# Performance work log

Measured on AMD Instinct MI355X. Metric: run time of the kernel, lower is better.

## Reference

```python
import jax, jax.numpy as jnp
import numpy as np

SEQ_LEN = 4096
INPUT_DIM = 768
DIM = 512
NUM_HEADS = 8
HEAD_DIM = DIM // NUM_HEADS
WINDOW_SIZE = 7
DILATION = 8
HALF_WINDOW = WINDOW_SIZE // 2  # 3
BIDIRECTIONAL = True


def _dilated_mask(seq_len):
    # allowed neighbors of query i: j = i + k*DILATION for k in [-HALF_WINDOW, HALF_WINDOW]
    # (only k<=0 if not bidirectional), clipped to [0, seq_len)
    idx = jnp.arange(seq_len)
    d = idx[None, :] - idx[:, None]  # j - i
    allowed = (d % DILATION == 0) & (jnp.abs(d) <= DILATION * HALF_WINDOW)
    if not BIDIRECTIONAL:
        allowed = allowed & (d <= 0)
    return jnp.where(allowed, 0.0, -jnp.inf).astype(jnp.float32)  # [S, S]


def setup_inputs() -> dict:
    key = jax.random.key(0)
    ks = jax.random.split(key, 6)
    s = 0.02
    return {
        "x": jax.random.normal(ks[0], (SEQ_LEN, INPUT_DIM), dtype=jnp.float32),
        "W_in": jax.random.normal(ks[1], (INPUT_DIM, DIM), dtype=jnp.float32) * s,
        "b_in": jnp.zeros((DIM,), dtype=jnp.float32),
        "W_tse": jax.random.normal(ks[2], (DIM, 3 * DIM), dtype=jnp.float32) * s,
        "W_out": jax.random.normal(ks[3], (DIM, DIM), dtype=jnp.float32) * s,
        "b_out": jnp.zeros((DIM,), dtype=jnp.float32),
    }


def reference(x, W_in, b_in, W_tse, W_out, b_out):
    S = x.shape[0]
    scale = HEAD_DIM ** -0.5
    h = x @ W_in + b_in                                   # [S, DIM]
    tse = (h @ W_tse).reshape(S, 3, NUM_HEADS, HEAD_DIM)   # [S, 3, H, hd]
    q, k, v = tse[:, 0], tse[:, 1], tse[:, 2]              # each [S, H, hd]
    scores = jnp.einsum("shd,thd->hst", q, k) * scale      # [H, S, S]
    scores = scores + _dilated_mask(S)[None, :, :]
    attn = jax.nn.softmax(scores, axis=-1)                 # [H, S, S]
    out = jnp.einsum("hst,thd->shd", attn, v)              # [S, H, hd]
    out = out.reshape(S, DIM)
    return out @ W_out + b_out                              # [S, DIM]
```

## Files before the change

kernel.cpp:

```cpp
#include <hip/hip_runtime.h>
#include <hip/hip_bf16.h>

#define S_LEN 4096
#define IN_DIM 768
#define D_DIM 512
#define N_HEADS 8
#define H_DIM 64
#define TSE_DIM 1536

typedef __attribute__((ext_vector_type(8))) short frag8;
typedef __attribute__((ext_vector_type(4))) float f32x4;

__device__ __forceinline__ unsigned short f2bfbits(float f) {
    unsigned int u = __float_as_uint(f);
    unsigned int r = (u + 0x7FFFu + ((u >> 16) & 1u)) >> 16;
    return (unsigned short)r;
}
__device__ __forceinline__ float bf2f(unsigned short b) {
    return __uint_as_float(((unsigned int)b) << 16);
}

__device__ __forceinline__ void gload_lds16(const void* g, void* l) {
    __builtin_amdgcn_global_load_lds(
        (const __attribute__((address_space(1))) unsigned int*)g,
        (__attribute__((address_space(3))) unsigned int*)l,
        16, 0, 0);
}

__global__ __launch_bounds__(256) void prep_kernel(
        const float4* __restrict__ x4, ushort4* __restrict__ xb4,
        const float* __restrict__ W_in,  unsigned short* __restrict__ WinT,
        const float* __restrict__ W_tse, unsigned short* __restrict__ WtseT,
        const float* __restrict__ W_out, unsigned short* __restrict__ WoutT) {
    __shared__ float tile[32][33];
    int b = blockIdx.x;
    if (b < 3072) {
        int i = b * 256 + threadIdx.x;
        float4 v = x4[i];
        ushort4 o;
        o.x = f2bfbits(v.x); o.y = f2bfbits(v.y);
        o.z = f2bfbits(v.z); o.w = f2bfbits(v.w);
        xb4[i] = o;
        return;
    }
    const float* in; unsigned short* out; int K, N, t;
    if (b < 3456)      { t = b - 3072; in = W_in;  out = WinT;  K = IN_DIM; N = D_DIM;  }
    else if (b < 4224) { t = b - 3456; in = W_tse; out = WtseT; K = D_DIM;  N = TSE_DIM;}
    else               { t = b - 4224; in = W_out; out = WoutT; K = D_DIM;  N = D_DIM;  }
    int ktiles = K / 32;
    int kb = (t % ktiles) * 32, nb = (t / ktiles) * 32;
    int tx = threadIdx.x & 31, ty = threadIdx.x >> 5;
    #pragma unroll
    for (int r = ty; r < 32; r += 8)
        tile[r][tx] = in[(size_t)(kb + r) * N + nb + tx];
    __syncthreads();
    #pragma unroll
    for (int r = ty; r < 32; r += 8)
        out[(size_t)(nb + r) * K + kb + tx] = f2bfbits(tile[tx][r]);
}

template<int NF, bool OUT_BF16, bool BIAS>
__global__ __launch_bounds__(256) void gemm_nt(
        const unsigned short* __restrict__ A,
        const unsigned short* __restrict__ Bt,
        const float* __restrict__ bias,
        void* __restrict__ C,
        int M, int N, int K) {
    constexpr int BN = 32 * NF;
    constexpr int BI = NF / 2;
    __shared__ __align__(16) unsigned short As[128 * 32];
    __shared__ __align__(16) unsigned short Bs[BN * 32];

    const int bm = blockIdx.x * 128;
    const int bn = blockIdx.y * BN;
    const int tid  = threadIdx.x;
    const int lane = tid & 63;
    const int wave = tid >> 6;
    const int wr = wave >> 1;
    const int wc = wave & 1;
    const int fr = lane & 15;
    const int fg = lane >> 4;

    const int srow = lane >> 2;
    const int scol = (lane & 3) * 8;

    const unsigned short* agp0 = A + (size_t)(bm + wave * 32 + srow) * K + scol;
    const unsigned short* agp1 = agp0 + (size_t)16 * K;
    unsigned short* alp0 = &As[(wave * 2) * 512];
    unsigned short* alp1 = alp0 + 512;

    const unsigned short* bgp[BI];
    unsigned short* blp[BI];
    #pragma unroll
    for (int r = 0; r < BI; ++r) {
        int ch = wave * BI + r;
        bgp[r] = Bt + (size_t)(bn + ch * 16 + srow) * K + scol;
        blp[r] = &Bs[ch * 512];
    }

    f32x4 acc[4][NF];
    #pragma unroll
    for (int mi = 0; mi < 4; ++mi)
        #pragma unroll
        for (int ni = 0; ni < NF; ++ni)
            acc[mi][ni] = (f32x4)(0.f);

    const int kTiles = K >> 5;
    for (int kt = 0; kt < kTiles; ++kt) {
        const int ko = kt << 5;
        gload_lds16(agp0 + ko, alp0);
        gload_lds16(agp1 + ko, alp1);
        #pragma unroll
        for (int r = 0; r < BI; ++r)
            gload_lds16(bgp[r] + ko, blp[r]);
        __syncthreads();

        frag8 a[4], b[NF];
        #pragma unroll
        for (int mi = 0; mi < 4; ++mi)
            a[mi] = *(const frag8*)&As[(wr * 64 + mi * 16 + fr) * 32 + fg * 8];
        #pragma unroll
        for (int ni = 0; ni < NF; ++ni)
            b[ni] = *(const frag8*)&Bs[(wc * (BN / 2) + ni * 16 + fr) * 32 + fg * 8];

        #pragma unroll
        for (int mi = 0; mi < 4; ++mi)
            #pragma unroll
            for (int ni = 0; ni < NF; ++ni)
                acc[mi][ni] = __builtin_amdgcn_mfma_f32_16x16x32_bf16(
                        a[mi], b[ni], acc[mi][ni], 0, 0, 0);
        __syncthreads();
    }

    #pragma unroll
    for (int mi = 0; mi < 4; ++mi) {
        int grow = bm + wr * 64 + mi * 16 + fg * 4;
        #pragma unroll
        for (int ni = 0; ni < NF; ++ni) {
            int gcol = bn + wc * (BN / 2) + ni * 16 + fr;
            float bv = BIAS ? bias[gcol] : 0.f;
            #pragma unroll
            for (int r = 0; r < 4; ++r) {
                float v = acc[mi][ni][r] + bv;
                if (OUT_BF16)
                    ((unsigned short*)C)[(size_t)(grow + r) * N + gcol] = f2bfbits(v);
                else
                    ((float*)C)[(size_t)(grow + r) * N + gcol] = v;
            }
        }
    }
}

__global__ __launch_bounds__(256) void attn_kernel(
        const unsigned short* __restrict__ tse, unsigned short* __restrict__ out) {
    const int s    = blockIdx.x * 4 + (threadIdx.x >> 6);
    const int lane = threadIdx.x & 63;
    const int off  = (lane >> 3) * H_DIM + (lane & 7) * 8;

    float qf[8];
    {
        frag8 q = *(const frag8*)(tse + (size_t)s * TSE_DIM + off);
        #pragma unroll
        for (int i = 0; i < 8; ++i) qf[i] = bf2f((unsigned short)q[i]);
    }

    float sc[7];
    #pragma unroll
    for (int j = 0; j < 7; ++j) {
        int t = s + (j - 3) * 8;
        bool valid = (t >= 0) && (t < S_LEN);
        float p = 0.f;
        if (valid) {
            frag8 k = *(const frag8*)(tse + (size_t)t * TSE_DIM + D_DIM + off);
            #pragma unroll
            for (int i = 0; i < 8; ++i) p += qf[i] * bf2f((unsigned short)k[i]);
        }
        p += __shfl_xor(p, 1, 64);
        p += __shfl_xor(p, 2, 64);
        p += __shfl_xor(p, 4, 64);
        sc[j] = valid ? p * 0.125f : -__builtin_inff();
    }

    float m = sc[0];
    #pragma unroll
    for (int j = 1; j < 7; ++j) m = fmaxf(m, sc[j]);

    float w[7], denom = 0.f;
    #pragma unroll
    for (int j = 0; j < 7; ++j) {
        w[j] = (sc[j] == -__builtin_inff()) ? 0.f : __expf(sc[j] - m);
        denom += w[j];
    }
    const float inv = 1.f / denom;

    float of[8];
    #pragma unroll
    for (int i = 0; i < 8; ++i) of[i] = 0.f;
    #pragma unroll
    for (int j = 0; j < 7; ++j) {
        int t = s + (j - 3) * 8;
        if (t >= 0 && t < S_LEN) {
            frag8 v = *(const frag8*)(tse + (size_t)t * TSE_DIM + 2 * D_DIM + off);
            #pragma unroll
            for (int i = 0; i < 8; ++i) of[i] += w[j] * bf2f((unsigned short)v[i]);
        }
    }

    frag8 o;
    #pragma unroll
    for (int i = 0; i < 8; ++i) o[i] = (short)f2bfbits(of[i] * inv);
    *(frag8*)(out + (size_t)s * D_DIM + off) = o;
}

extern "C" void kernel_launch(void* const* d_in, const int* in_sizes, int n_in,
                              void* d_out, int out_size, void* d_ws, size_t ws_size,
                              hipStream_t stream) {
    (void)in_sizes; (void)n_in; (void)out_size;
    const float* x     = (const float*)d_in[0];
    const float* W_in  = (const float*)d_in[1];
    const float* b_in  = (const float*)d_in[2];
    const float* W_tse = (const float*)d_in[3];
    const float* W_out = (const float*)d_in[4];
    const float* b_out = (const float*)d_in[5];

    char* p = (char*)d_ws;
    unsigned short* xb    = (unsigned short*)p; p += (size_t)S_LEN * IN_DIM * 2;
    unsigned short* WinT  = (unsigned short*)p; p += (size_t)D_DIM * IN_DIM * 2;
    unsigned short* WtseT = (unsigned short*)p; p += (size_t)TSE_DIM * D_DIM * 2;
    unsigned short* WoutT = (unsigned short*)p; p += (size_t)D_DIM * D_DIM * 2;
    unsigned short* h     = (unsigned short*)p; p += (size_t)S_LEN * D_DIM * 2;
    unsigned short* tse   = (unsigned short*)p; p += (size_t)S_LEN * TSE_DIM * 2;
    unsigned short* attn  = (unsigned short*)p; p += (size_t)S_LEN * D_DIM * 2;
    if ((size_t)(p - (char*)d_ws) > ws_size) return;

    prep_kernel<<<4480, 256, 0, stream>>>(
            (const float4*)x, (ushort4*)xb, W_in, WinT, W_tse, WtseT, W_out, WoutT);

    gemm_nt<2, true, true><<<dim3(S_LEN / 128, D_DIM / 64), 256, 0, stream>>>(
            xb, WinT, b_in, h, S_LEN, D_DIM, IN_DIM);
    gemm_nt<4, true, false><<<dim3(S_LEN / 128, TSE_DIM / 128), 256, 0, stream>>>(
            h, WtseT, nullptr, tse, S_LEN, TSE_DIM, D_DIM);
    attn_kernel<<<S_LEN / 4, 256, 0, stream>>>(tse, attn);
    gemm_nt<2, false, true><<<dim3(S_LEN / 128, D_DIM / 64), 256, 0, stream>>>(
            attn, WoutT, b_out, (float*)d_out, S_LEN, D_DIM, D_DIM);
}
```

Before: 62.74 us.

## Use 64x64 GEMM tiles with double-buffered LDS prefetch

Replaces the templated 128xBN GEMM with a fixed 64x64 tile whose LDS buffers are double-buffered, so the global-to-LDS load of the next K tile is issued before the MFMAs on the current one. Smaller tiles give more blocks to fill the many CUs for these modest sizes (512 blocks for the 512-wide GEMMs), and there is one barrier per K step instead of two. The cost is less reuse per block: more global and L2 traffic and fewer MFMAs per loaded byte. Correctness relies on the barrier at the end of each iteration both making the prefetched tile visible and stopping the other buffer from being overwritten while it is still being read.

```diff
diff --git a/kernel.cpp b/kernel.cpp
--- a/kernel.cpp
+++ b/kernel.cpp
@@ -59,23 +59,20 @@
         out[(size_t)(nb + r) * K + kb + tx] = f2bfbits(tile[tx][r]);
 }
 
-template<int NF, bool OUT_BF16, bool BIAS>
+template<bool OUT_BF16, bool BIAS>
 __global__ __launch_bounds__(256) void gemm_nt(
         const unsigned short* __restrict__ A,
         const unsigned short* __restrict__ Bt,
         const float* __restrict__ bias,
         void* __restrict__ C,
         int M, int N, int K) {
-    constexpr int BN = 32 * NF;
-    constexpr int BI = NF / 2;
-    __shared__ __align__(16) unsigned short As[128 * 32];
-    __shared__ __align__(16) unsigned short Bs[BN * 32];
-
-    const int bm = blockIdx.x * 128;
-    const int bn = blockIdx.y * BN;
-    const int tid  = threadIdx.x;
-    const int lane = tid & 63;
-    const int wave = tid >> 6;
+    __shared__ __align__(16) unsigned short As[2][64 * 32];
+    __shared__ __align__(16) unsigned short Bs[2][64 * 32];
+
+    const int bm = blockIdx.x * 64;
+    const int bn = blockIdx.y * 64;
+    const int lane = threadIdx.x & 63;
+    const int wave = threadIdx.x >> 6;
     const int wr = wave >> 1;
     const int wc = wave & 1;
     const int fr = lane & 15;
@@ -84,60 +81,72 @@
     const int srow = lane >> 2;
     const int scol = (lane & 3) * 8;
 
-    const unsigned short* agp0 = A + (size_t)(bm + wave * 32 + srow) * K + scol;
-    const unsigned short* agp1 = agp0 + (size_t)16 * K;
-    unsigned short* alp0 = &As[(wave * 2) * 512];
-    unsigned short* alp1 = alp0 + 512;
-
-    const unsigned short* bgp[BI];
-    unsigned short* blp[BI];
-    #pragma unroll
-    for (int r = 0; r < BI; ++r) {
-        int ch = wave * BI + r;
-        bgp[r] = Bt + (size_t)(bn + ch * 16 + srow) * K + scol;
-        blp[r] = &Bs[ch * 512];
-    }
-
-    f32x4 acc[4][NF];
-    #pragma unroll
-    for (int mi = 0; mi < 4; ++mi)
-        #pragma unroll
-        for (int ni = 0; ni < NF; ++ni)
+    const unsigned short* agp = A  + (size_t)(bm + wave * 16 + srow) * K + scol;
+    const unsigned short* bgp = Bt + (size_t)(bn + wave * 16 + srow) * K + scol;
+    unsigned short* alp0 = &As[0][wave * 512];
+    unsigned short* blp0 = &Bs[0][wave * 512];
+    unsigned short* alp1 = &As[1][wave * 512];
+    unsigned short* blp1 = &Bs[1][wave * 512];
+
+    f32x4 acc[2][2];
+    #pragma unroll
+    for (int mi = 0; mi < 2; ++mi)
+        #pragma unroll
+        for (int ni = 0; ni < 2; ++ni)
             acc[mi][ni] = (f32x4)(0.f);
 
-    const int kTiles = K >> 5;
-    for (int kt = 0; kt < kTiles; ++kt) {
-        const int ko = kt << 5;
-        gload_lds16(agp0 + ko, alp0);
-        gload_lds16(agp1 + ko, alp1);
-        #pragma unroll
-        for (int r = 0; r < BI; ++r)
-            gload_lds16(bgp[r] + ko, blp[r]);
-        __syncthreads();
-
-        frag8 a[4], b[NF];
-        #pragma unroll
-        for (int mi = 0; mi < 4; ++mi)
-            a[mi] = *(const frag8*)&As[(wr * 64 + mi * 16 + fr) * 32 + fg * 8];
-        #pragma unroll
-        for (int ni = 0; ni < NF; ++ni)
-            b[ni] = *(const frag8*)&Bs[(wc * (BN / 2) + ni * 16 + fr) * 32 + fg * 8];
-
-        #pragma unroll
-        for (int mi = 0; mi < 4; ++mi)
-            #pragma unroll
-            for (int ni = 0; ni < NF; ++ni)
+    const int nt = K >> 5;
+
+    gload_lds16(agp, alp0);
+    gload_lds16(bgp, blp0);
+    __syncthreads();
+
+    int cur = 0;
+    for (int kt = 0; kt + 1 < nt; ++kt) {
+        const int ko = (kt + 1) << 5;
+        gload_lds16(agp + ko, cur ? alp0 : alp1);
+        gload_lds16(bgp + ko, cur ? blp0 : blp1);
+
+        frag8 a[2], b[2];
+        #pragma unroll
+        for (int mi = 0; mi < 2; ++mi)
+            a[mi] = *(const frag8*)&As[cur][(wr * 32 + mi * 16 + fr) * 32 + fg * 8];
+        #pragma unroll
+        for (int ni = 0; ni < 2; ++ni)
+            b[ni] = *(const frag8*)&Bs[cur][(wc * 32 + ni * 16 + fr) * 32 + fg * 8];
+        #pragma unroll
+        for (int mi = 0; mi < 2; ++mi)
+            #pragma unroll
+            for (int ni = 0; ni < 2; ++ni)
                 acc[mi][ni] = __builtin_amdgcn_mfma_f32_16x16x32_bf16(
                         a[mi], b[ni], acc[mi][ni], 0, 0, 0);
+
         __syncthreads();
-    }
-
-    #pragma unroll
-    for (int mi = 0; mi < 4; ++mi) {
-        int grow = bm + wr * 64 + mi * 16 + fg * 4;
-        #pragma unroll
-        for (int ni = 0; ni < NF; ++ni) {
-            int gcol = bn + wc * (BN / 2) + ni * 16 + fr;
+        cur ^= 1;
+    }
+
+    {
+        frag8 a[2], b[2];
+        #pragma unroll
+        for (int mi = 0; mi < 2; ++mi)
+            a[mi] = *(const frag8*)&As[cur][(wr * 32 + mi * 16 + fr) * 32 + fg * 8];
+        #pragma unroll
+        for (int ni = 0; ni < 2; ++ni)
+            b[ni] = *(const frag8*)&Bs[cur][(wc * 32 + ni * 16 + fr) * 32 + fg * 8];
+        #pragma unroll
+        for (int mi = 0; mi < 2; ++mi)
+            #pragma unroll
+            for (int ni = 0; ni < 2; ++ni)
+                acc[mi][ni] = __builtin_amdgcn_mfma_f32_16x16x32_bf16(
+                        a[mi], b[ni], acc[mi][ni], 0, 0, 0);
+    }
+
+    #pragma unroll
+    for (int mi = 0; mi < 2; ++mi) {
+        int grow = bm + wr * 32 + mi * 16 + fg * 4;
+        #pragma unroll
+        for (int ni = 0; ni < 2; ++ni) {
+            int gcol = bn + wc * 32 + ni * 16 + fr;
             float bv = BIAS ? bias[gcol] : 0.f;
             #pragma unroll
             for (int r = 0; r < 4; ++r) {
@@ -236,11 +245,11 @@
     prep_kernel<<<4480, 256, 0, stream>>>(
             (const float4*)x, (ushort4*)xb, W_in, WinT, W_tse, WtseT, W_out, WoutT);
 
-    gemm_nt<2, true, true><<<dim3(S_LEN / 128, D_DIM / 64), 256, 0, stream>>>(
+    gemm_nt<true, true><<<dim3(S_LEN / 64, D_DIM / 64), 256, 0, stream>>>(
             xb, WinT, b_in, h, S_LEN, D_DIM, IN_DIM);
-    gemm_nt<4, true, false><<<dim3(S_LEN / 128, TSE_DIM / 128), 256, 0, stream>>>(
+    gemm_nt<true, false><<<dim3(S_LEN / 64, TSE_DIM / 64), 256, 0, stream>>>(
             h, WtseT, nullptr, tse, S_LEN, TSE_DIM, D_DIM);
     attn_kernel<<<S_LEN / 4, 256, 0, stream>>>(tse, attn);
-    gemm_nt<2, false, true><<<dim3(S_LEN / 128, D_DIM / 64), 256, 0, stream>>>(
+    gemm_nt<false, true><<<dim3(S_LEN / 64, D_DIM / 64), 256, 0, stream>>>(
             attn, WoutT, b_out, (float*)d_out, S_LEN, D_DIM, D_DIM);
 }
```

Result: faster. 53.03 us (-15.5%).

## Double-buffer GEMM LDS tiles and shrink block tiles for more blocks

Applied to the files above, without the earlier changes.

The GEMM kernel now keeps two LDS buffers and issues the global-to-LDS loads for the next K tile before running MFMAs on the current one, so there is one barrier per iteration instead of two. The M tile is also a template parameter. The 768- and 512-K GEMMs now use 64x64 tiles and the QKV GEMM uses 128x64, which raises the block count from 256-384 to 512-768 to fill the CUs better. The cost is more LDS per block, less operand reuse per block, and more redundant global traffic.

```diff
diff --git a/kernel.cpp b/kernel.cpp
--- a/kernel.cpp
+++ b/kernel.cpp
@@ -59,23 +59,23 @@
         out[(size_t)(nb + r) * K + kb + tx] = f2bfbits(tile[tx][r]);
 }
 
-template<int NF, bool OUT_BF16, bool BIAS>
+template<int MF, int NF, bool OUT_BF16, bool BIAS>
 __global__ __launch_bounds__(256) void gemm_nt(
         const unsigned short* __restrict__ A,
         const unsigned short* __restrict__ Bt,
         const float* __restrict__ bias,
         void* __restrict__ C,
         int M, int N, int K) {
-    constexpr int BN = 32 * NF;
+    constexpr int BM = MF * 32, BN = NF * 32;
+    constexpr int AI = MF / 2;
     constexpr int BI = NF / 2;
-    __shared__ __align__(16) unsigned short As[128 * 32];
-    __shared__ __align__(16) unsigned short Bs[BN * 32];
-
-    const int bm = blockIdx.x * 128;
+    __shared__ __align__(16) unsigned short As[2][BM * 32];
+    __shared__ __align__(16) unsigned short Bs[2][BN * 32];
+
+    const int bm = blockIdx.x * BM;
     const int bn = blockIdx.y * BN;
-    const int tid  = threadIdx.x;
-    const int lane = tid & 63;
-    const int wave = tid >> 6;
+    const int lane = threadIdx.x & 63;
+    const int wave = threadIdx.x >> 6;
     const int wr = wave >> 1;
     const int wc = wave & 1;
     const int fr = lane & 15;
@@ -84,57 +84,78 @@
     const int srow = lane >> 2;
     const int scol = (lane & 3) * 8;
 
-    const unsigned short* agp0 = A + (size_t)(bm + wave * 32 + srow) * K + scol;
-    const unsigned short* agp1 = agp0 + (size_t)16 * K;
-    unsigned short* alp0 = &As[(wave * 2) * 512];
-    unsigned short* alp1 = alp0 + 512;
-
+    const unsigned short* agp[AI];
     const unsigned short* bgp[BI];
-    unsigned short* blp[BI];
-    #pragma unroll
-    for (int r = 0; r < BI; ++r) {
-        int ch = wave * BI + r;
-        bgp[r] = Bt + (size_t)(bn + ch * 16 + srow) * K + scol;
-        blp[r] = &Bs[ch * 512];
-    }
-
-    f32x4 acc[4][NF];
-    #pragma unroll
-    for (int mi = 0; mi < 4; ++mi)
+    #pragma unroll
+    for (int r = 0; r < AI; ++r)
+        agp[r] = A + (size_t)(bm + (wave * AI + r) * 16 + srow) * K + scol;
+    #pragma unroll
+    for (int r = 0; r < BI; ++r)
+        bgp[r] = Bt + (size_t)(bn + (wave * BI + r) * 16 + srow) * K + scol;
+
+    f32x4 acc[MF][NF];
+    #pragma unroll
+    for (int mi = 0; mi < MF; ++mi)
         #pragma unroll
         for (int ni = 0; ni < NF; ++ni)
             acc[mi][ni] = (f32x4)(0.f);
 
-    const int kTiles = K >> 5;
-    for (int kt = 0; kt < kTiles; ++kt) {
-        const int ko = kt << 5;
-        gload_lds16(agp0 + ko, alp0);
-        gload_lds16(agp1 + ko, alp1);
+    const int nt = K >> 5;
+
+    #pragma unroll
+    for (int r = 0; r < AI; ++r) gload_lds16(agp[r], &As[0][(wave * AI + r) * 512]);
+    #pragma unroll
+    for (int r = 0; r < BI; ++r) gload_lds16(bgp[r], &Bs[0][(wave * BI + r) * 512]);
+    __syncthreads();
+
+    int cur = 0;
+    for (int kt = 0; kt + 1 < nt; ++kt) {
+        const int ko = (kt + 1) << 5;
+        const int nb = cur ^ 1;
+        #pragma unroll
+        for (int r = 0; r < AI; ++r)
+            gload_lds16(agp[r] + ko, &As[nb][(wave * AI + r) * 512]);
         #pragma unroll
         for (int r = 0; r < BI; ++r)
-            gload_lds16(bgp[r] + ko, blp[r]);
-        __syncthreads();
-
-        frag8 a[4], b[NF];
-        #pragma unroll
-        for (int mi = 0; mi < 4; ++mi)
-            a[mi] = *(const frag8*)&As[(wr * 64 + mi * 16 + fr) * 32 + fg * 8];
+            gload_lds16(bgp[r] + ko, &Bs[nb][(wave * BI + r) * 512]);
+
+        frag8 a[MF], b[NF];
+        #pragma unroll
+        for (int mi = 0; mi < MF; ++mi)
+            a[mi] = *(const frag8*)&As[cur][(wr * (BM / 2) + mi * 16 + fr) * 32 + fg * 8];
         #pragma unroll
         for (int ni = 0; ni < NF; ++ni)
-            b[ni] = *(const frag8*)&Bs[(wc * (BN / 2) + ni * 16 + fr) * 32 + fg * 8];
-
-        #pragma unroll
-        for (int mi = 0; mi < 4; ++mi)
+            b[ni] = *(const frag8*)&Bs[cur][(wc * (BN / 2) + ni * 16 + fr) * 32 + fg * 8];
+        #pragma unroll
+        for (int mi = 0; mi < MF; ++mi)
             #pragma unroll
             for (int ni = 0; ni < NF; ++ni)
                 acc[mi][ni] = __builtin_amdgcn_mfma_f32_16x16x32_bf16(
                         a[mi], b[ni], acc[mi][ni], 0, 0, 0);
+
         __syncthreads();
-    }
-
-    #pragma unroll
-    for (int mi = 0; mi < 4; ++mi) {
-        int grow = bm + wr * 64 + mi * 16 + fg * 4;
+        cur ^= 1;
+    }
+
+    {
+        frag8 a[MF], b[NF];
+        #pragma unroll
+        for (int mi = 0; mi < MF; ++mi)
+            a[mi] = *(const frag8*)&As[cur][(wr * (BM / 2) + mi * 16 + fr) * 32 + fg * 8];
+        #pragma unroll
+        for (int ni = 0; ni < NF; ++ni)
+            b[ni] = *(const frag8*)&Bs[cur][(wc * (BN / 2) + ni * 16 + fr) * 32 + fg * 8];
+        #pragma unroll
+        for (int mi = 0; mi < MF; ++mi)
+            #pragma unroll
+            for (int ni = 0; ni < NF; ++ni)
+                acc[mi][ni] = __builtin_amdgcn_mfma_f32_16x16x32_bf16(
+                        a[mi], b[ni], acc[mi][ni], 0, 0, 0);
+    }
+
+    #pragma unroll
+    for (int mi = 0; mi < MF; ++mi) {
+        int grow = bm + wr * (BM / 2) + mi * 16 + fg * 4;
         #pragma unroll
         for (int ni = 0; ni < NF; ++ni) {
             int gcol = bn + wc * (BN / 2) + ni * 16 + fr;
@@ -236,11 +257,11 @@
     prep_kernel<<<4480, 256, 0, stream>>>(
             (const float4*)x, (ushort4*)xb, W_in, WinT, W_tse, WtseT, W_out, WoutT);
 
-    gemm_nt<2, true, true><<<dim3(S_LEN / 128, D_DIM / 64), 256, 0, stream>>>(
+    gemm_nt<2, 2, true, true><<<dim3(S_LEN / 64, D_DIM / 64), 256, 0, stream>>>(
             xb, WinT, b_in, h, S_LEN, D_DIM, IN_DIM);
-    gemm_nt<4, true, false><<<dim3(S_LEN / 128, TSE_DIM / 128), 256, 0, stream>>>(
+    gemm_nt<4, 2, true, false><<<dim3(S_LEN / 128, TSE_DIM / 64), 256, 0, stream>>>(
             h, WtseT, nullptr, tse, S_LEN, TSE_DIM, D_DIM);
     attn_kernel<<<S_LEN / 4, 256, 0, stream>>>(tse, attn);
-    gemm_nt<2, false, true><<<dim3(S_LEN / 128, D_DIM / 64), 256, 0, stream>>>(
+    gemm_nt<2, 2, false, true><<<dim3(S_LEN / 64, D_DIM / 64), 256, 0, stream>>>(
             attn, WoutT, b_out, (float*)d_out, S_LEN, D_DIM, D_DIM);
 }
```

After: 55.37 us. 1.13x faster.
